# Optimization experiments

Measured on AMD Instinct MI355X. Metric: run time of the kernel, lower is better.

Reference implementation:

```python
import jax, jax.numpy as jnp
import numpy as np

B, CIN, COUT, HID, H, W, K, PAD = 16, 64, 64, 32, 32, 32, 5, 2


def self_attention(x, Wq, Wk, Wv):
    # x: [B,C,H,W]; Wq,Wk: [HID,C]; Wv: [C,C]  (1x1 convs as channel matmuls)
    b, c, h, w = x.shape
    n = h * w
    xf = x.reshape(b, c, n)                      # [B,C,N]
    q = jnp.einsum('dc,bcn->bdn', Wq, xf)        # [B,HID,N]
    k = jnp.einsum('dc,bcn->bdn', Wk, xf)        # [B,HID,N]
    v = jnp.einsum('ec,bcn->ben', Wv, xf)        # [B,C,N]
    scores = jnp.einsum('bdn,bdm->bnm', q, k)    # [B,N,N]
    attn = jax.nn.softmax(scores, axis=-1)
    out = jnp.einsum('bcm,bnm->bcn', v, attn)    # aggregate values
    out = out.reshape(b, c, h, w)
    return x + out, attn                          # residual


def conv_lstm_cell(x, h, c, W_lstm, b_lstm):
    combined = jnp.concatenate([x, h], axis=1)   # [B,CIN+COUT,H,W]
    gates = jax.lax.conv_general_dilated(
        combined, W_lstm, window_strides=(1, 1),
        padding=[(PAD, PAD), (PAD, PAD)],
        dimension_numbers=('NCHW', 'OIHW', 'NCHW'))
    gates = gates + b_lstm[None, :, None, None]
    i, f, o, g = jnp.split(gates, 4, axis=1)
    i, f, o = jax.nn.sigmoid(i), jax.nn.sigmoid(f), jax.nn.sigmoid(o)
    g = jnp.tanh(g)
    c_new = f * c + i * g
    h_new = o * jnp.tanh(c_new)
    return h_new, c_new


def setup_inputs() -> dict:
    key = jax.random.key(0)
    ks = jax.random.split(key, 12)
    s = 0.05
    return {
        'x': jax.random.normal(ks[0], (B, CIN, H, W), jnp.float32),
        'h': jax.random.normal(ks[1], (B, COUT, H, W), jnp.float32),
        'c': jax.random.normal(ks[2], (B, COUT, H, W), jnp.float32),
        'Wq_x': jax.random.normal(ks[3], (HID, CIN), jnp.float32) * s,
        'Wk_x': jax.random.normal(ks[4], (HID, CIN), jnp.float32) * s,
        'Wv_x': jax.random.normal(ks[5], (CIN, CIN), jnp.float32) * s,
        'Wq_h': jax.random.normal(ks[6], (HID, COUT), jnp.float32) * s,
        'Wk_h': jax.random.normal(ks[7], (HID, COUT), jnp.float32) * s,
        'Wv_h': jax.random.normal(ks[8], (COUT, COUT), jnp.float32) * s,
        'W_lstm': jax.random.normal(ks[9], (4 * COUT, CIN + COUT, K, K), jnp.float32) * s,
        'b_lstm': jnp.zeros((4 * COUT,), jnp.float32),
    }


def reference(x, h, c, Wq_x, Wk_x, Wv_x, Wq_h, Wk_h, Wv_h, W_lstm, b_lstm):
    X, _ = self_attention(x, Wq_x, Wk_x, Wv_x)
    new_h, new_c = conv_lstm_cell(X, h, c, W_lstm, b_lstm)
    new_h, atten = self_attention(new_h, Wq_h, Wk_h, Wv_h)
    new_h = new_h + new_h  # faithful to `new_h += new_h`
    return new_h, new_c, atten
```

## Files before the change

### kernel.cpp

```cpp
#include <hip/hip_runtime.h>
#include <hip/hip_bf16.h>
#include <cstddef>
#include <cstdint>

#define NTOK 1024
#define NB   16
#define NC   64
#define NHID 32

#define PAD_BSTRIDE 165888
#define PAD_KSTRIDE 82944
#define PAD_BYTES   5308416

typedef __attribute__((ext_vector_type(8))) short short8;
typedef __attribute__((ext_vector_type(4))) float f32x4;

__device__ __forceinline__ ushort f2b(float f) {
  uint32_t u = __builtin_bit_cast(uint32_t, f);
  return (ushort)((u + 0x7FFFu + ((u >> 16) & 1u)) >> 16);
}
__device__ __forceinline__ float b2f(ushort u) {
  return __builtin_bit_cast(float, (uint32_t)u << 16);
}
__device__ __forceinline__ short8 ldw8(const float* __restrict__ p) {
  float4 f0 = *(const float4*)p, f1 = *(const float4*)(p + 4);
  short8 r;
  r[0] = (short)f2b(f0.x); r[1] = (short)f2b(f0.y);
  r[2] = (short)f2b(f0.z); r[3] = (short)f2b(f0.w);
  r[4] = (short)f2b(f1.x); r[5] = (short)f2b(f1.y);
  r[6] = (short)f2b(f1.z); r[7] = (short)f2b(f1.w);
  return r;
}
__device__ __forceinline__ float sigm(float x) { return 1.f / (1.f + __expf(-x)); }
__device__ __forceinline__ float tanh_fast(float x) {
  float e = __expf(2.f * x);
  return 1.f - 2.f / (e + 1.f);
}

__global__ __launch_bounds__(256) void tpose_pad_kernel(
    const float* __restrict__ src, ushort* __restrict__ dst) {
  __shared__ float tile[64][65];
  int t = threadIdx.x;
  int n0 = blockIdx.x * 64, b = blockIdx.y;
  const float* s = src + (size_t)b * NC * NTOK;
#pragma unroll
  for (int r = 0; r < 4; ++r) {
    int c = r * 16 + (t >> 4);
    int nl = (t & 15) * 4;
    float4 v = *(const float4*)(s + (size_t)c * NTOK + n0 + nl);
    tile[c][nl] = v.x; tile[c][nl + 1] = v.y; tile[c][nl + 2] = v.z; tile[c][nl + 3] = v.w;
  }
  __syncthreads();
  int tok = t >> 2, c0 = (t & 3) * 16;
  __attribute__((aligned(16))) ushort tmp[16];
#pragma unroll
  for (int i = 0; i < 16; ++i) tmp[i] = f2b(tile[c0 + i][tok]);
  int gtok = n0 + tok;
  ushort* d = dst + (size_t)b * PAD_BSTRIDE +
              ((gtok >> 5) + 2) * 2304 + ((gtok & 31) + 2) * 64 + c0;
  *(uint4*)(d)     = *(const uint4*)(tmp);
  *(uint4*)(d + 8) = *(const uint4*)(tmp + 8);
}

__global__ __launch_bounds__(256) void qkvproj_kernel(
    const float* __restrict__ x, const float* __restrict__ Wq,
    const float* __restrict__ Wk, const float* __restrict__ Wv,
    ushort* __restrict__ qT, ushort* __restrict__ kT, ushort* __restrict__ vb) {
  __shared__ float tile[64][65];
  __shared__ ushort xb[64][72];
  __shared__ ushort sq[64][32], sk[64][32];
  int t = threadIdx.x, wave = t >> 6, lane = t & 63;
  int lo = lane & 15, lg = lane >> 4;
  int n0 = blockIdx.x * 64, b = blockIdx.y;
  const float* s = x + (size_t)b * NC * NTOK;
#pragma unroll
  for (int r = 0; r < 4; ++r) {
    int c = r * 16 + (t >> 4);
    int nl = (t & 15) * 4;
    float4 v = *(const float4*)(s + (size_t)c * NTOK + n0 + nl);
    tile[c][nl] = v.x; tile[c][nl + 1] = v.y; tile[c][nl + 2] = v.z; tile[c][nl + 3] = v.w;
  }
  __syncthreads();
  {
    int tok = t >> 2, c0 = (t & 3) * 16;
    __attribute__((aligned(16))) ushort tmp[16];
#pragma unroll
    for (int i = 0; i < 16; ++i) tmp[i] = f2b(tile[c0 + i][tok]);
    *(uint4*)(&xb[tok][c0])     = *(const uint4*)(tmp);
    *(uint4*)(&xb[tok][c0 + 8]) = *(const uint4*)(tmp + 8);
  }
  __syncthreads();
  const ushort* xrow = &xb[wave * 16 + lo][8 * lg];
  short8 a0 = *(const short8*)(xrow);
  short8 a1 = *(const short8*)(xrow + 32);
  f32x4 aq[2], ak[2];
#pragma unroll
  for (int dg = 0; dg < 2; ++dg) {
    short8 wq0 = ldw8(Wq + (size_t)(dg * 16 + lo) * NC + 8 * lg);
    short8 wq1 = ldw8(Wq + (size_t)(dg * 16 + lo) * NC + 32 + 8 * lg);
    short8 wk0 = ldw8(Wk + (size_t)(dg * 16 + lo) * NC + 8 * lg);
    short8 wk1 = ldw8(Wk + (size_t)(dg * 16 + lo) * NC + 32 + 8 * lg);
    f32x4 z = {0.f, 0.f, 0.f, 0.f};
    aq[dg] = __builtin_amdgcn_mfma_f32_16x16x32_bf16(a0, wq0, z, 0, 0, 0);
    aq[dg] = __builtin_amdgcn_mfma_f32_16x16x32_bf16(a1, wq1, aq[dg], 0, 0, 0);
    ak[dg] = __builtin_amdgcn_mfma_f32_16x16x32_bf16(a0, wk0, z, 0, 0, 0);
    ak[dg] = __builtin_amdgcn_mfma_f32_16x16x32_bf16(a1, wk1, ak[dg], 0, 0, 0);
  }
  f32x4 av[4];
#pragma unroll
  for (int g = 0; g < 4; ++g) {
    short8 wv0 = ldw8(Wv + (size_t)(g * 16 + lo) * NC + 8 * lg);
    short8 wv1 = ldw8(Wv + (size_t)(g * 16 + lo) * NC + 32 + 8 * lg);
    f32x4 z = {0.f, 0.f, 0.f, 0.f};
    av[g] = __builtin_amdgcn_mfma_f32_16x16x32_bf16(wv0, a0, z, 0, 0, 0);
    av[g] = __builtin_amdgcn_mfma_f32_16x16x32_bf16(wv1, a1, av[g], 0, 0, 0);
  }
#pragma unroll
  for (int dg = 0; dg < 2; ++dg)
#pragma unroll
    for (int r = 0; r < 4; ++r) {
      sq[wave * 16 + 4 * lg + r][dg * 16 + lo] = f2b(aq[dg][r]);
      sk[wave * 16 + 4 * lg + r][dg * 16 + lo] = f2b(ak[dg][r]);
    }
  ushort* vbase = vb + (size_t)b * NC * NTOK + n0 + wave * 16 + lo;
#pragma unroll
  for (int g = 0; g < 4; ++g)
#pragma unroll
    for (int r = 0; r < 4; ++r)
      vbase[(size_t)(g * 16 + lg * 4 + r) * NTOK] = f2b(av[g][r]);
  __syncthreads();
  int tok = t >> 2, d0 = (t & 3) * 8;
  size_t base = ((size_t)b * NTOK + n0 + tok) * NHID + d0;
  *(short8*)(qT + base) = *(const short8*)(&sq[tok][d0]);
  *(short8*)(kT + base) = *(const short8*)(&sk[tok][d0]);
}

#define SP 1048
template <bool ATTN2>
__global__ __launch_bounds__(256) void attn_fused_kernel(
    const ushort* __restrict__ qT, const ushort* __restrict__ kT,
    const ushort* __restrict__ vb, const float* __restrict__ resid,
    float* __restrict__ attnf, float* __restrict__ outf,
    ushort* __restrict__ outb_pad, float scale) {
  __shared__ ushort s_lds[16 * SP];
  __shared__ float wmax[4][16], wsum[4][16];
  int t = threadIdx.x, wave = t >> 6, lane = t & 63;
  int lo = lane & 15, lg = lane >> 4;
  int n0 = blockIdx.x * 16, b = blockIdx.y;
  int m0 = wave * 256;
  short8 a = *(const short8*)(qT + ((size_t)b * NTOK + n0 + lo) * NHID + 8 * lg);
  f32x4 acc[16];
#pragma unroll
  for (int j = 0; j < 16; ++j) {
    short8 bf = *(const short8*)(kT + ((size_t)b * NTOK + m0 + j * 16 + lo) * NHID + 8 * lg);
    f32x4 z = {0.f, 0.f, 0.f, 0.f};
    acc[j] = __builtin_amdgcn_mfma_f32_16x16x32_bf16(a, bf, z, 0, 0, 0);
  }
  float pm[4];
#pragma unroll
  for (int r = 0; r < 4; ++r) {
    float m = acc[0][r];
#pragma unroll
    for (int j = 1; j < 16; ++j) m = fmaxf(m, acc[j][r]);
#pragma unroll
    for (int off = 1; off < 16; off <<= 1) m = fmaxf(m, __shfl_xor(m, off, 64));
    pm[r] = m;
  }
  if (lo == 0)
#pragma unroll
    for (int r = 0; r < 4; ++r) wmax[wave][4 * lg + r] = pm[r];
  __syncthreads();
  float mr[4];
#pragma unroll
  for (int r = 0; r < 4; ++r)
    mr[r] = fmaxf(fmaxf(wmax[0][4 * lg + r], wmax[1][4 * lg + r]),
                  fmaxf(wmax[2][4 * lg + r], wmax[3][4 * lg + r]));
  float ps[4] = {0.f, 0.f, 0.f, 0.f};
#pragma unroll
  for (int j = 0; j < 16; ++j)
#pragma unroll
    for (int r = 0; r < 4; ++r) {
      float e = __expf(acc[j][r] - mr[r]);
      acc[j][r] = e;
      ps[r] += e;
    }
#pragma unroll
  for (int r = 0; r < 4; ++r)
#pragma unroll
    for (int off = 1; off < 16; off <<= 1) ps[r] += __shfl_xor(ps[r], off, 64);
  if (lo == 0)
#pragma unroll
    for (int r = 0; r < 4; ++r) wsum[wave][4 * lg + r] = ps[r];
  __syncthreads();
  float inv[4];
#pragma unroll
  for (int r = 0; r < 4; ++r)
    inv[r] = 1.f / (wsum[0][4 * lg + r] + wsum[1][4 * lg + r] +
                    wsum[2][4 * lg + r] + wsum[3][4 * lg + r]);
#pragma unroll
  for (int j = 0; j < 16; ++j)
#pragma unroll
    for (int r = 0; r < 4; ++r)
      s_lds[(4 * lg + r) * SP + m0 + j * 16 + lo] = f2b(acc[j][r] * inv[r]);
  __syncthreads();
  if constexpr (ATTN2) {
    int ml = lane * 4;
    float* abase = attnf + ((size_t)b * NTOK + n0) * NTOK + m0;
#pragma unroll
    for (int n = 0; n < 16; ++n) {
      ushort4 sv = *(const ushort4*)(s_lds + n * SP + m0 + ml);
      float4 o;
      o.x = b2f(sv.x); o.y = b2f(sv.y); o.z = b2f(sv.z); o.w = b2f(sv.w);
      *(float4*)(abase + (size_t)n * NTOK + ml) = o;
    }
  }
  int cb = wave * 16;
  const ushort* vbb = vb + ((size_t)b * NC + cb + lo) * NTOK;
  f32x4 acc2 = {0.f, 0.f, 0.f, 0.f}, acc3 = {0.f, 0.f, 0.f, 0.f};
  for (int ms = 0; ms < NTOK; ms += 64) {
    short8 af0 = *(const short8*)(s_lds + lo * SP + ms + 8 * lg);
    short8 bf0 = *(const short8*)(vbb + ms + 8 * lg);
    short8 af1 = *(const short8*)(s_lds + lo * SP + ms + 32 + 8 * lg);
    short8 bf1 = *(const short8*)(vbb + ms + 32 + 8 * lg);
    acc2 = __builtin_amdgcn_mfma_f32_16x16x32_bf16(af0, bf0, acc2, 0, 0, 0);
    acc3 = __builtin_amdgcn_mfma_f32_16x16x32_bf16(af1, bf1, acc3, 0, 0, 0);
  }
#pragma unroll
  for (int r = 0; r < 4; ++r) acc2[r] += acc3[r];
  int c = cb + lo;
  float4 rv = *(const float4*)(resid + ((size_t)b * NC + c) * NTOK + n0 + 4 * lg);
  float rvv[4] = {rv.x, rv.y, rv.z, rv.w};
  if constexpr (ATTN2) {
    float4 o;
    o.x = scale * (rvv[0] + acc2[0]); o.y = scale * (rvv[1] + acc2[1]);
    o.z = scale * (rvv[2] + acc2[2]); o.w = scale * (rvv[3] + acc2[3]);
    *(float4*)(outf + ((size_t)b * NC + c) * NTOK + n0 + 4 * lg) = o;
  } else {
#pragma unroll
    for (int r = 0; r < 4; ++r) {
      int tok = n0 + 4 * lg + r;
      float val = scale * (rvv[r] + acc2[r]);
      outb_pad[(size_t)b * PAD_BSTRIDE + ((tok >> 5) + 2) * 2304 +
               ((tok & 31) + 2) * 64 + c] = f2b(val);
    }
  }
}

__global__ __launch_bounds__(256) void wpre_kernel(
    const float* __restrict__ W, ushort* __restrict__ Wb) {
  int idx = blockIdx.x * 256 + threadIdx.x;
  const float* src = W + (size_t)idx * 25;
#pragma unroll
  for (int kk = 0; kk < 25; ++kk)
    Wb[((size_t)(idx >> 7) * 25 + kk) * 128 + (idx & 127)] = f2b(src[kk]);
}

#define AP 76
#define BP 76
__global__ __launch_bounds__(512, 1) void conv_lstm_kernel(
    const ushort* __restrict__ pad,
    const ushort* __restrict__ Wb,
    const float* __restrict__ bias, const float* __restrict__ c_in,
    float* __restrict__ c_out, float* __restrict__ h_out) {
  __shared__ ushort ldsA[2][256 * AP];
  __shared__ ushort ldsB[432 * BP];
  int t = threadIdx.x;
  int lane = t & 63, lo = lane & 15, lg = lane >> 4;
  int wid = t >> 6, ocr_base = (wid & 3) * 16, ph = wid >> 2;
  int pt = blockIdx.x, b = blockIdx.y;
  {
    const ushort* pb = pad + (size_t)b * PAD_BSTRIDE + (size_t)(pt * 2) * 2304;
    for (int i = t; i < 432 * 8; i += 512) {
      int pxw = i >> 3, ch8 = (i & 7) * 8;
      int kh = pxw >= 216, w = pxw - kh * 216;
      uint4 v = *(const uint4*)(pb + (size_t)kh * PAD_KSTRIDE + w * 64 + ch8);
      *(uint4*)(ldsB + pxw * BP + ch8) = v;
    }
  }
  const ushort *wsrc0, *wsrc1, *wsrc2, *wsrc3;
  int adst0, adst1, adst2, adst3;
  {
    int i0 = t, i1 = 512 + t, i2 = 1024 + t, i3 = 1536 + t;
    wsrc0 = Wb + (size_t)(i0 >> 3) * 3200 + (i0 & 7) * 8;
    wsrc1 = Wb + (size_t)(i1 >> 3) * 3200 + (i1 & 7) * 8;
    wsrc2 = Wb + (size_t)(i2 >> 3) * 3200 + (i2 & 7) * 8;
    wsrc3 = Wb + (size_t)(i3 >> 3) * 3200 + (i3 & 7) * 8;
    adst0 = (i0 >> 3) * AP + (i0 & 7) * 8;
    adst1 = (i1 >> 3) * AP + (i1 & 7) * 8;
    adst2 = (i2 >> 3) * AP + (i2 & 7) * 8;
    adst3 = (i3 >> 3) * AP + (i3 & 7) * 8;
  }
  uint4 w0 = *(const uint4*)(wsrc0);
  uint4 w1 = *(const uint4*)(wsrc1);
  uint4 w2 = *(const uint4*)(wsrc2);
  uint4 w3 = *(const uint4*)(wsrc3);

  f32x4 acc[4][2];
#pragma unroll
  for (int i = 0; i < 4; ++i)
#pragma unroll
    for (int j = 0; j < 2; ++j) acc[i][j] = {0.f, 0.f, 0.f, 0.f};

  __syncthreads();
  *(uint4*)(&ldsA[0][adst0]) = w0;
  *(uint4*)(&ldsA[0][adst1]) = w1;
  *(uint4*)(&ldsA[0][adst2]) = w2;
  *(uint4*)(&ldsA[0][adst3]) = w3;
  w0 = *(const uint4*)(wsrc0 + 128);
  w1 = *(const uint4*)(wsrc1 + 128);
  w2 = *(const uint4*)(wsrc2 + 128);
  w3 = *(const uint4*)(wsrc3 + 128);
  __syncthreads();

  for (int s = 0; s < 50; ++s) {
    int cur = s & 1;
    if (s < 49) {
      int nxt = cur ^ 1;
      *(uint4*)(&ldsA[nxt][adst0]) = w0;
      *(uint4*)(&ldsA[nxt][adst1]) = w1;
      *(uint4*)(&ldsA[nxt][adst2]) = w2;
      *(uint4*)(&ldsA[nxt][adst3]) = w3;
      int s2 = (s < 48) ? s + 2 : 49;
      int koff = (s2 < 25) ? s2 * 128 : (s2 - 25) * 128 + 64;
      w0 = *(const uint4*)(wsrc0 + koff);
      w1 = *(const uint4*)(wsrc1 + koff);
      w2 = *(const uint4*)(wsrc2 + koff);
      w3 = *(const uint4*)(wsrc3 + koff);
    }
    int kh = (s >= 25);
    int tap = s - kh * 25;
    int ky = tap / 5, kx = tap - 5 * ky;
    int bbase = (kh * 216 + ky * 36 + kx) * BP;
#pragma unroll
    for (int icc = 0; icc < 2; ++icc) {
      short8 af[4], bf[2];
#pragma unroll
      for (int i = 0; i < 4; ++i)
        af[i] = *(const short8*)(&ldsA[cur][(i * 64 + ocr_base + lo) * AP + icc * 32 + 8 * lg]);
#pragma unroll
      for (int j = 0; j < 2; ++j)
        bf[j] = *(const short8*)(ldsB + bbase + (ph * 36 + j * 16 + lo) * BP + icc * 32 + 8 * lg);
#pragma unroll
      for (int i = 0; i < 4; ++i)
#pragma unroll
        for (int j = 0; j < 2; ++j)
          acc[i][j] = __builtin_amdgcn_mfma_f32_16x16x32_bf16(af[i], bf[j], acc[i][j], 0, 0, 0);
    }
    __syncthreads();
  }

#pragma unroll
  for (int j = 0; j < 2; ++j)
#pragma unroll
    for (int r = 0; r < 4; ++r) {
      int ocr = ocr_base + lg * 4 + r;
      int p = pt * 64 + ph * 32 + j * 16 + lo;
      size_t ci = ((size_t)b * NC + ocr) * NTOK + p;
      float iv = sigm(acc[0][j][r] + bias[ocr]);
      float fv = sigm(acc[1][j][r] + bias[64 + ocr]);
      float ov = sigm(acc[2][j][r] + bias[128 + ocr]);
      float gv = tanh_fast(acc[3][j][r] + bias[192 + ocr]);
      float cn = fv * c_in[ci] + iv * gv;
      c_out[ci] = cn;
      h_out[ci] = ov * tanh_fast(cn);
    }
}

extern "C" void kernel_launch(void* const* d_in, const int* in_sizes, int n_in,
                              void* d_out, int out_size, void* d_ws, size_t ws_size,
                              hipStream_t stream) {
  const float* x      = (const float*)d_in[0];
  const float* h      = (const float*)d_in[1];
  const float* c      = (const float*)d_in[2];
  const float* Wq_x   = (const float*)d_in[3];
  const float* Wk_x   = (const float*)d_in[4];
  const float* Wv_x   = (const float*)d_in[5];
  const float* Wq_h   = (const float*)d_in[6];
  const float* Wk_h   = (const float*)d_in[7];
  const float* Wv_h   = (const float*)d_in[8];
  const float* W_lstm = (const float*)d_in[9];
  const float* b_lstm = (const float*)d_in[10];

  float* out   = (float*)d_out;
  float* new_h = out;
  float* new_c = out + 1048576;
  float* atten = out + 2097152;

  ushort* wsu = (ushort*)d_ws;
  ushort* qT  = wsu;
  ushort* kT  = wsu + 524288;
  ushort* vb  = wsu + 1048576;

  ushort* Wb    = (ushort*)(atten + 8388608);
  ushort* pad   = (ushort*)(atten + 9437184);
  float*  h_mid = new_h;

  dim3 blk(256);
  hipMemsetAsync(pad, 0, PAD_BYTES, stream);
  qkvproj_kernel<<<dim3(16, NB), blk, 0, stream>>>(x, Wq_x, Wk_x, Wv_x, qT, kT, vb);
  attn_fused_kernel<false><<<dim3(64, NB), blk, 0, stream>>>(
      qT, kT, vb, x, nullptr, nullptr, pad , 1.0f);
  wpre_kernel<<<128, blk, 0, stream>>>(W_lstm, Wb);
  tpose_pad_kernel<<<dim3(16, NB), blk, 0, stream>>>(h, pad + PAD_KSTRIDE);
  conv_lstm_kernel<<<dim3(16, NB), 512, 0, stream>>>(pad, Wb, b_lstm, c, new_c, h_mid);
  qkvproj_kernel<<<dim3(16, NB), blk, 0, stream>>>(h_mid, Wq_h, Wk_h, Wv_h, qT, kT, vb);
  attn_fused_kernel<true><<<dim3(64, NB), blk, 0, stream>>>(
      qT, kT, vb, h_mid, atten, new_h, nullptr, 2.0f);
}
```

Baseline: 129.5 us.

## Split conv-LSTM blocks across output-channel halves and reload input tile mid-loop

```diff
diff --git a/kernel.cpp b/kernel.cpp
--- a/kernel.cpp
+++ b/kernel.cpp
@@ -257,38 +257,38 @@
 
 #define AP 76
 #define BP 76
-__global__ __launch_bounds__(512, 1) void conv_lstm_kernel(
+__global__ __launch_bounds__(256, 2) void conv_lstm_kernel(
     const ushort* __restrict__ pad,
     const ushort* __restrict__ Wb,
     const float* __restrict__ bias, const float* __restrict__ c_in,
     float* __restrict__ c_out, float* __restrict__ h_out) {
-  __shared__ ushort ldsA[2][256 * AP];
-  __shared__ ushort ldsB[432 * BP];
+  __shared__ ushort ldsA[2][128 * AP];
+  __shared__ ushort ldsB[216 * BP];
   int t = threadIdx.x;
   int lane = t & 63, lo = lane & 15, lg = lane >> 4;
-  int wid = t >> 6, ocr_base = (wid & 3) * 16, ph = wid >> 2;
-  int pt = blockIdx.x, b = blockIdx.y;
-  {
-    const ushort* pb = pad + (size_t)b * PAD_BSTRIDE + (size_t)(pt * 2) * 2304;
-    for (int i = t; i < 432 * 8; i += 512) {
-      int pxw = i >> 3, ch8 = (i & 7) * 8;
-      int kh = pxw >= 216, w = pxw - kh * 216;
-      uint4 v = *(const uint4*)(pb + (size_t)kh * PAD_KSTRIDE + w * 64 + ch8);
-      *(uint4*)(ldsB + pxw * BP + ch8) = v;
-    }
-  }
+  int wid = t >> 6, cb = wid & 1, ph = wid >> 1;
+  int pt = blockIdx.x, chh = blockIdx.y, b = blockIdx.z;
+  const ushort* pb = pad + (size_t)b * PAD_BSTRIDE + (size_t)(pt * 2) * 2304;
+
+  for (int i = t; i < 1728; i += 256) {
+    int pxw = i >> 3, ch8 = (i & 7) * 8;
+    uint4 v = *(const uint4*)(pb + (size_t)pxw * 64 + ch8);
+    *(uint4*)(ldsB + pxw * BP + ch8) = v;
+  }
+
   const ushort *wsrc0, *wsrc1, *wsrc2, *wsrc3;
   int adst0, adst1, adst2, adst3;
   {
-    int i0 = t, i1 = 512 + t, i2 = 1024 + t, i3 = 1536 + t;
-    wsrc0 = Wb + (size_t)(i0 >> 3) * 3200 + (i0 & 7) * 8;
-    wsrc1 = Wb + (size_t)(i1 >> 3) * 3200 + (i1 & 7) * 8;
-    wsrc2 = Wb + (size_t)(i2 >> 3) * 3200 + (i2 & 7) * 8;
-    wsrc3 = Wb + (size_t)(i3 >> 3) * 3200 + (i3 & 7) * 8;
-    adst0 = (i0 >> 3) * AP + (i0 & 7) * 8;
-    adst1 = (i1 >> 3) * AP + (i1 & 7) * 8;
-    adst2 = (i2 >> 3) * AP + (i2 & 7) * 8;
-    adst3 = (i3 >> 3) * AP + (i3 & 7) * 8;
+    int i0 = t, i1 = 256 + t, i2 = 512 + t, i3 = 768 + t;
+    int r0 = i0 >> 3, r1 = i1 >> 3, r2 = i2 >> 3, r3 = i3 >> 3;
+    wsrc0 = Wb + (size_t)((r0 >> 5) * 64 + chh * 32 + (r0 & 31)) * 3200 + (i0 & 7) * 8;
+    wsrc1 = Wb + (size_t)((r1 >> 5) * 64 + chh * 32 + (r1 & 31)) * 3200 + (i1 & 7) * 8;
+    wsrc2 = Wb + (size_t)((r2 >> 5) * 64 + chh * 32 + (r2 & 31)) * 3200 + (i2 & 7) * 8;
+    wsrc3 = Wb + (size_t)((r3 >> 5) * 64 + chh * 32 + (r3 & 31)) * 3200 + (i3 & 7) * 8;
+    adst0 = r0 * AP + (i0 & 7) * 8;
+    adst1 = r1 * AP + (i1 & 7) * 8;
+    adst2 = r2 * AP + (i2 & 7) * 8;
+    adst3 = r3 * AP + (i3 & 7) * 8;
   }
   uint4 w0 = *(const uint4*)(wsrc0);
   uint4 w1 = *(const uint4*)(wsrc1);
@@ -330,13 +330,13 @@
     int kh = (s >= 25);
     int tap = s - kh * 25;
     int ky = tap / 5, kx = tap - 5 * ky;
-    int bbase = (kh * 216 + ky * 36 + kx) * BP;
+    int bbase = (ky * 36 + kx) * BP;
 #pragma unroll
     for (int icc = 0; icc < 2; ++icc) {
       short8 af[4], bf[2];
 #pragma unroll
       for (int i = 0; i < 4; ++i)
-        af[i] = *(const short8*)(&ldsA[cur][(i * 64 + ocr_base + lo) * AP + icc * 32 + 8 * lg]);
+        af[i] = *(const short8*)(&ldsA[cur][(i * 32 + cb * 16 + lo) * AP + icc * 32 + 8 * lg]);
 #pragma unroll
       for (int j = 0; j < 2; ++j)
         bf[j] = *(const short8*)(ldsB + bbase + (ph * 36 + j * 16 + lo) * BP + icc * 32 + 8 * lg);
@@ -347,19 +347,27 @@
           acc[i][j] = __builtin_amdgcn_mfma_f32_16x16x32_bf16(af[i], bf[j], acc[i][j], 0, 0, 0);
     }
     __syncthreads();
+    if (s == 24) {
+      for (int i = t; i < 1728; i += 256) {
+        int pxw = i >> 3, ch8 = (i & 7) * 8;
+        uint4 v = *(const uint4*)(pb + PAD_KSTRIDE + (size_t)pxw * 64 + ch8);
+        *(uint4*)(ldsB + pxw * BP + ch8) = v;
+      }
+      __syncthreads();
+    }
   }
 
 #pragma unroll
   for (int j = 0; j < 2; ++j)
 #pragma unroll
     for (int r = 0; r < 4; ++r) {
-      int ocr = ocr_base + lg * 4 + r;
+      int ch = chh * 32 + cb * 16 + lg * 4 + r;
       int p = pt * 64 + ph * 32 + j * 16 + lo;
-      size_t ci = ((size_t)b * NC + ocr) * NTOK + p;
-      float iv = sigm(acc[0][j][r] + bias[ocr]);
-      float fv = sigm(acc[1][j][r] + bias[64 + ocr]);
-      float ov = sigm(acc[2][j][r] + bias[128 + ocr]);
-      float gv = tanh_fast(acc[3][j][r] + bias[192 + ocr]);
+      size_t ci = ((size_t)b * NC + ch) * NTOK + p;
+      float iv = sigm(acc[0][j][r] + bias[ch]);
+      float fv = sigm(acc[1][j][r] + bias[64 + ch]);
+      float ov = sigm(acc[2][j][r] + bias[128 + ch]);
+      float gv = tanh_fast(acc[3][j][r] + bias[192 + ch]);
       float cn = fv * c_in[ci] + iv * gv;
       c_out[ci] = cn;
       h_out[ci] = ov * tanh_fast(cn);
@@ -402,7 +410,7 @@
       qT, kT, vb, x, nullptr, nullptr, pad , 1.0f);
   wpre_kernel<<<128, blk, 0, stream>>>(W_lstm, Wb);
   tpose_pad_kernel<<<dim3(16, NB), blk, 0, stream>>>(h, pad + PAD_KSTRIDE);
-  conv_lstm_kernel<<<dim3(16, NB), 512, 0, stream>>>(pad, Wb, b_lstm, c, new_c, h_mid);
+  conv_lstm_kernel<<<dim3(16, 2, NB), blk, 0, stream>>>(pad, Wb, b_lstm, c, new_c, h_mid);
   qkvproj_kernel<<<dim3(16, NB), blk, 0, stream>>>(h_mid, Wq_h, Wk_h, Wv_h, qT, kT, vb);
   attn_fused_kernel<true><<<dim3(64, NB), blk, 0, stream>>>(
       qT, kT, vb, h_mid, atten, new_h, nullptr, 2.0f);
```

After: 127.7 us. About the same (-1.4%).
